# Performance work log

Hardware: AMD Instinct MI355X
Metric: run time of the kernel (lower is better)

Reference implementation:

```python
import jax, jax.numpy as jnp
import numpy as np

B, N, C, IN, H, G, OUT = 128, 256, 4, 64, 128, 8, 1
NUM_GNN_LAYERS = 2  # num_layers - 1


def setup_inputs() -> dict:
    key = jax.random.key(0)
    k1, k2, k3, k4, k5, k6 = jax.random.split(key, 6)
    V = jax.random.normal(k1, (B, N, IN), dtype=jnp.float32)
    A = jax.random.uniform(k2, (B, N, C, N), dtype=jnp.float32)
    mol_size = jax.random.randint(k3, (B,), 16, N + 1)  # at least 16 real nodes
    W_in = jax.random.normal(k4, (2, H, IN, G), dtype=jnp.float32) / np.float32(np.sqrt(IN) * np.sqrt(G))
    W_g = jax.random.normal(k5, (NUM_GNN_LAYERS, 2, H, H, G), dtype=jnp.float32) / np.float32(np.sqrt(H) * np.sqrt(G))
    W_out = jax.random.normal(k6, (2, OUT, H, 1), dtype=jnp.float32) / np.float32(np.sqrt(H))
    b_out = jnp.zeros((1, OUT), dtype=jnp.float32)
    return {"V": V, "A": A, "mol_size": mol_size, "W_in": W_in, "W_g": W_g, "W_out": W_out, "b_out": b_out}


def _kan_linear(x, W, bias=None):
    # x: [..., in], W: [2, out, in, grid]
    g = W.shape[-1]
    k = jnp.arange(1, g + 1, dtype=x.dtype)  # [g]
    xk = x[..., None] * k                    # [..., in, g]
    y = jnp.einsum('...ik,oik->...o', jnp.cos(xk), W[0]) \
      + jnp.einsum('...ik,oik->...o', jnp.sin(xk), W[1])
    if bias is not None:
        y = y + bias
    return y


def _kan_gnn_layer(h, A, W):
    # h: [b,n,in], A: [b,n,c,m], W: [2,out,in,grid]
    g = W.shape[-1]
    k = jnp.arange(1, g + 1, dtype=h.dtype)
    xk = h[..., None] * k                      # [b,n,in,g]
    f = jnp.einsum('bnik,oik->bno', jnp.cos(xk), W[0]) \
      + jnp.einsum('bnik,oik->bno', jnp.sin(xk), W[1])  # fourier_feat [b,n,out]
    # torch chain permute/reshape/bmm/sum(c) == sum_{n,c} A[b,n,c,m] * f[b,n,o]
    return jnp.einsum('bncm,bno->bmo', A, f)   # [b,m,out]


def reference(V, A, mol_size, W_in, W_g, W_out, b_out):
    h = _kan_linear(V, W_in)                   # [B,N,H]
    for i in range(W_g.shape[0]):
        m = _kan_gnn_layer(h, A, W_g[i])
        h = jax.nn.leaky_relu(m + h, negative_slope=0.01)
    # avg pooling over the first mol_size[i] (real) nodes per graph
    node_mask = (jnp.arange(N) < mol_size[:, None]).astype(h.dtype)  # [B,N]
    summed = jnp.einsum('bnh,bn->bh', h, node_mask)
    y = summed / mol_size[:, None].astype(h.dtype)                    # [B,H]
    out = jax.nn.sigmoid(_kan_linear(y, W_out, b_out))                # [B,OUT]
    return out
```

## Files before the change

### kernel.cpp

```cpp
#include <hip/hip_runtime.h>
#include <math.h>

namespace {
constexpr int B_ = 128;
constexpr int N_ = 256;
constexpr int H_ = 128;
constexpr int M_TOTAL = B_ * N_;
}

#define AS1 __attribute__((address_space(1)))
#define AS3 __attribute__((address_space(3)))

__device__ __forceinline__ void gl_lds16(const float* g, float* l) {
  __builtin_amdgcn_global_load_lds((const AS1 unsigned int*)g,
                                   (AS3 unsigned int*)l, 16, 0, 0);
}

template<int I, int O>
__global__ __launch_bounds__(256)
void wtr_kernel(const float* __restrict__ in, float* __restrict__ out) {
  int idx = blockIdx.x * 256 + threadIdx.x;
  constexpr int TOTAL = 2 * O * I * 8;
  if (idx >= TOTAL) return;
  int g = idx & 7;
  int t = idx >> 3;
  int i = t % I;
  int t2 = t / I;
  int o = t2 % O;
  int s = t2 / O;
  out[(size_t)((i * 8 + g) * 2 + s) * O + o] = in[idx];
}

__global__ __launch_bounds__(256)
void add4_kernel(const float* __restrict__ a, const float* __restrict__ b,
                 float* __restrict__ o, int n4) {
  int i = blockIdx.x * 256 + threadIdx.x;
  int stride = gridDim.x * 256;
  for (; i < n4; i += stride) {
    float4 x = ((const float4*)a)[i];
    float4 y = ((const float4*)b)[i];
    float4 r = {x.x + y.x, x.y + y.y, x.z + y.z, x.w + y.w};
    ((float4*)o)[i] = r;
  }
}

template<int IN>
__global__ __launch_bounds__(256, 4)
void fourier4(const float* __restrict__ x,
              const float* __restrict__ Wt,
              float* __restrict__ out0,
              float* __restrict__ out1)
{
  constexpr int HP = IN * 4;
  constexpr int CHUNKS = HP / 8;
  __shared__ alignas(16) float wl[2][8][2][128];
  __shared__ alignas(16) float fC[2][8][64];
  __shared__ alignas(16) float fS[2][8][64];

  const int tid = threadIdx.x;
  const int khalf = blockIdx.x & 1;
  const int node0 = (blockIdx.x >> 1) * 64;
  const int og = tid & 15;
  const int ng = tid >> 4;
  const int lane = tid & 63;
  const int wave = tid >> 6;
  const int nd = tid & 63;

  float* __restrict__ out = khalf ? out1 : out0;
  const float* wb = Wt + (size_t)khalf * HP * 256;
  const float* xrow = x + (size_t)(node0 + nd) * IN + khalf * (IN / 2);

  float acc[4][8];
  #pragma unroll
  for (int a = 0; a < 4; ++a)
    #pragma unroll
    for (int b = 0; b < 8; ++b) acc[a][b] = 0.f;

  float xv = xrow[0];
  float xnext = (CHUNKS > 1) ? xrow[1] : 0.f;
  #pragma unroll
  for (int q = 0; q < 2; ++q) {
    int bw = wave * 2 + q;
    gl_lds16(wb + (size_t)(bw * 64 + lane) * 4, &wl[0][0][0][0] + bw * 256);
  }
  {
    float s1, c1;
    sincosf(xv, &s1, &c1);
    float ckm = 1.f, skm = 0.f, ck = c1, sk = s1;
    #pragma unroll
    for (int g = 0; g < 8; ++g) {
      if ((g >> 1) == wave) { fC[0][g][nd] = ck; fS[0][g][nd] = sk; }
      float cn = 2.f * c1 * ck - ckm, sn = 2.f * c1 * sk - skm;
      ckm = ck; skm = sk; ck = cn; sk = sn;
    }
  }
  __syncthreads();

  int p = 0;
  for (int ic = 0; ic < CHUNKS; ++ic) {
    const int pn = p ^ 1;
    const bool more = (ic + 1 < CHUNKS);
    if (more) {
      const float* wsrc = wb + (size_t)(ic + 1) * 2048;
      #pragma unroll
      for (int q = 0; q < 2; ++q) {
        int bw = wave * 2 + q;
        gl_lds16(wsrc + (size_t)(bw * 64 + lane) * 4,
                 &wl[pn][0][0][0] + bw * 256);
      }
      float s1, c1;
      sincosf(xnext, &s1, &c1);
      float ckm = 1.f, skm = 0.f, ck = c1, sk = s1;
      #pragma unroll
      for (int g = 0; g < 8; ++g) {
        if ((g >> 1) == wave) { fC[pn][g][nd] = ck; fS[pn][g][nd] = sk; }
        float cn = 2.f * c1 * ck - ckm, sn = 2.f * c1 * sk - skm;
        ckm = ck; skm = sk; ck = cn; sk = sn;
      }
      if (ic + 2 < CHUNKS) xnext = xrow[ic + 2];
    }
    #pragma unroll 4
    for (int j = 0; j < 8; ++j) {
      float4 fc = *(const float4*)&fC[p][j][ng * 4];
      float4 fs = *(const float4*)&fS[p][j][ng * 4];
      float4 w0a = *(const float4*)&wl[p][j][0][og * 4];
      float4 w0b = *(const float4*)&wl[p][j][0][og * 4 + 64];
      float4 w1a = *(const float4*)&wl[p][j][1][og * 4];
      float4 w1b = *(const float4*)&wl[p][j][1][og * 4 + 64];
      float fcv[4] = {fc.x, fc.y, fc.z, fc.w};
      float fsv[4] = {fs.x, fs.y, fs.z, fs.w};
      float wa0[4] = {w0a.x, w0a.y, w0a.z, w0a.w};
      float wb0[4] = {w0b.x, w0b.y, w0b.z, w0b.w};
      float wa1[4] = {w1a.x, w1a.y, w1a.z, w1a.w};
      float wb1[4] = {w1b.x, w1b.y, w1b.z, w1b.w};
      #pragma unroll
      for (int nd2 = 0; nd2 < 4; ++nd2) {
        #pragma unroll
        for (int oo = 0; oo < 4; ++oo) {
          acc[nd2][oo]     += fcv[nd2] * wa0[oo] + fsv[nd2] * wa1[oo];
          acc[nd2][4 + oo] += fcv[nd2] * wb0[oo] + fsv[nd2] * wb1[oo];
        }
      }
    }
    __syncthreads();
    p ^= 1;
  }

  #pragma unroll
  for (int nd2 = 0; nd2 < 4; ++nd2) {
    int row = node0 + ng * 4 + nd2;
    float4 ra = {acc[nd2][0], acc[nd2][1], acc[nd2][2], acc[nd2][3]};
    float4 rb = {acc[nd2][4], acc[nd2][5], acc[nd2][6], acc[nd2][7]};
    *(float4*)&out[(size_t)row * H_ + og * 4] = ra;
    *(float4*)&out[(size_t)row * H_ + og * 4 + 64] = rb;
  }
}

__global__ __launch_bounds__(256)
void agg3(const float* __restrict__ A,
          const float* __restrict__ f0,
          const float* __restrict__ f1,
          const float* __restrict__ h_in,
          float* __restrict__ h_out)
{
  __shared__ alignas(16) float As[2][32][64];
  __shared__ alignas(16) float fsh[2][8][128];
  const int tid = threadIdx.x;
  const int b = blockIdx.x >> 2;
  const int m0 = (blockIdx.x & 3) * 64;
  const int og = tid & 15;
  const int mg = tid >> 4;
  const int wave = tid >> 6;
  const int fr = tid >> 5;
  const int fc4 = (tid & 31) * 4;

  float acc[4][8];
  #pragma unroll
  for (int i = 0; i < 4; ++i)
    #pragma unroll
    for (int j = 0; j < 8; ++j) acc[i][j] = 0.f;

  const float* Ab  = A  + (size_t)b * (N_ * 4 * N_) + m0;
  const float* f0b = f0 + (size_t)b * (N_ * H_);
  const float* f1b = f1 + (size_t)b * (N_ * H_);

  float4 u0 = *(const float4*)(f0b + (size_t)fr * H_ + fc4);
  float4 u1 = *(const float4*)(f1b + (size_t)fr * H_ + fc4);
  #pragma unroll
  for (int q = 0; q < 2; ++q) {
    int v = q * 256 + tid;
    gl_lds16(Ab + (size_t)(v >> 4) * N_ + (v & 15) * 4,
             &As[0][0][0] + (size_t)(q * 256 + wave * 64) * 4);
  }
  {
    float4 s = {u0.x + u1.x, u0.y + u1.y, u0.z + u1.z, u0.w + u1.w};
    *(float4*)&fsh[0][fr][fc4] = s;
  }
  __syncthreads();

  int p = 0;
  for (int ch = 0; ch < 32; ++ch) {
    const int pn = p ^ 1;
    float4 v0, v1;
    if (ch + 1 < 32) {
      v0 = *(const float4*)(f0b + (size_t)((ch + 1) * 8 + fr) * H_ + fc4);
      v1 = *(const float4*)(f1b + (size_t)((ch + 1) * 8 + fr) * H_ + fc4);
      const float* Asrc = Ab + (size_t)(ch + 1) * 32 * N_;
      #pragma unroll
      for (int q = 0; q < 2; ++q) {
        int v = q * 256 + tid;
        gl_lds16(Asrc + (size_t)(v >> 4) * N_ + (v & 15) * 4,
                 &As[pn][0][0] + (size_t)(q * 256 + wave * 64) * 4);
      }
    }
    #pragma unroll
    for (int kk = 0; kk < 32; ++kk) {
      float4 a  = *(const float4*)&As[p][kk][mg * 4];
      float4 g0 = *(const float4*)&fsh[p][kk >> 2][og * 4];
      float4 g1 = *(const float4*)&fsh[p][kk >> 2][og * 4 + 64];
      float av[4] = {a.x, a.y, a.z, a.w};
      float fo[8] = {g0.x, g0.y, g0.z, g0.w, g1.x, g1.y, g1.z, g1.w};
      #pragma unroll
      for (int mi = 0; mi < 4; ++mi)
        #pragma unroll
        for (int oi = 0; oi < 8; ++oi)
          acc[mi][oi] += av[mi] * fo[oi];
    }
    if (ch + 1 < 32) {
      float4 s = {v0.x + v1.x, v0.y + v1.y, v0.z + v1.z, v0.w + v1.w};
      *(float4*)&fsh[pn][fr][fc4] = s;
    }
    __syncthreads();
    p ^= 1;
  }

  #pragma unroll
  for (int mi = 0; mi < 4; ++mi) {
    int row = b * N_ + m0 + mg * 4 + mi;
    const float* hr = &h_in[(size_t)row * H_];
    float* ho = &h_out[(size_t)row * H_];
    float4 r0 = *(const float4*)&hr[og * 4];
    float4 r1 = *(const float4*)&hr[og * 4 + 64];
    float4 o0, o1;
    float v;
    v = acc[mi][0] + r0.x; o0.x = v >= 0.f ? v : 0.01f * v;
    v = acc[mi][1] + r0.y; o0.y = v >= 0.f ? v : 0.01f * v;
    v = acc[mi][2] + r0.z; o0.z = v >= 0.f ? v : 0.01f * v;
    v = acc[mi][3] + r0.w; o0.w = v >= 0.f ? v : 0.01f * v;
    v = acc[mi][4] + r1.x; o1.x = v >= 0.f ? v : 0.01f * v;
    v = acc[mi][5] + r1.y; o1.y = v >= 0.f ? v : 0.01f * v;
    v = acc[mi][6] + r1.z; o1.z = v >= 0.f ? v : 0.01f * v;
    v = acc[mi][7] + r1.w; o1.w = v >= 0.f ? v : 0.01f * v;
    *(float4*)&ho[og * 4] = o0;
    *(float4*)&ho[og * 4 + 64] = o1;
  }
}

__global__ __launch_bounds__(128)
void pool_kernel(const float* __restrict__ h,
                 const int* __restrict__ mol,
                 const float* __restrict__ Wout,
                 const float* __restrict__ bout,
                 float* __restrict__ out)
{
  __shared__ float red[128];
  const int b = blockIdx.x;
  const int t = threadIdx.x;
  const int ms = mol[b];
  const float* hb = h + (size_t)b * N_ * H_;
  float sum = 0.f;
  for (int n = 0; n < ms; ++n) sum += hb[(size_t)n * H_ + t];
  float y = sum / (float)ms;
  float s1, c1;
  sincosf(y, &s1, &c1);
  red[t] = c1 * Wout[t] + s1 * Wout[H_ + t];
  __syncthreads();
  for (int sft = 64; sft > 0; sft >>= 1) {
    if (t < sft) red[t] += red[t + sft];
    __syncthreads();
  }
  if (t == 0) {
    float z = red[0] + bout[0];
    out[b] = 1.f / (1.f + expf(-z));
  }
}

extern "C" void kernel_launch(void* const* d_in, const int* in_sizes, int n_in,
                              void* d_out, int out_size, void* d_ws, size_t ws_size,
                              hipStream_t stream) {
  const float* V    = (const float*)d_in[0];
  const float* A    = (const float*)d_in[1];
  const int*   mol  = (const int*)d_in[2];
  const float* Win  = (const float*)d_in[3];
  const float* Wg   = (const float*)d_in[4];
  const float* Wout = (const float*)d_in[5];
  const float* bout = (const float*)d_in[6];
  float* out = (float*)d_out;

  const size_t BUF = (size_t)M_TOTAL * H_;
  float* h     = (float*)d_ws;
  float* h2    = h  + BUF;
  float* f0    = h2 + BUF;
  float* f1    = f0 + BUF;
  float* wt_in = f1 + BUF;
  float* wt_g0 = wt_in + 512 * 2 * H_;
  float* wt_g1 = wt_g0 + 1024 * 2 * H_;

  wtr_kernel<64, 128><<<(2 * 128 * 64 * 8) / 256, 256, 0, stream>>>(Win, wt_in);
  wtr_kernel<128, 128><<<(2 * 128 * 128 * 8) / 256, 256, 0, stream>>>(Wg, wt_g0);
  wtr_kernel<128, 128><<<(2 * 128 * 128 * 8) / 256, 256, 0, stream>>>(
      Wg + (size_t)2 * 128 * 128 * 8, wt_g1);

  fourier4<64><<<(M_TOTAL / 64) * 2, 256, 0, stream>>>(V, wt_in, f0, f1);
  add4_kernel<<<2048, 256, 0, stream>>>(f0, f1, h, (int)(BUF / 4));

  float* hc = h;
  float* hn = h2;
  const float* wt_g[2] = {wt_g0, wt_g1};
  for (int l = 0; l < 2; ++l) {
    fourier4<128><<<(M_TOTAL / 64) * 2, 256, 0, stream>>>(hc, wt_g[l], f0, f1);
    agg3<<<B_ * 4, 256, 0, stream>>>(A, f0, f1, hc, hn);
    float* tmp = hc; hc = hn; hn = tmp;
  }

  pool_kernel<<<B_, 128, 0, stream>>>(hc, mol, Wout, bout, out);
}
```

Measured before the change: 1.006 ms.

## Enlarge per-thread register tiles to 8x8 in fourier and aggregation kernels

The Fourier feature GEMM kernel now covers 128 nodes per block, giving each thread an 8x8 accumulator tile instead of 4x8. Feature generation is split across two thread halves, with the upper half reaching harmonic 5 through angle doubling. The aggregation kernel uses 128 threads per block, and each thread computes 8 rows by 8 outputs, reusing each loaded f vector across four A rows. The goal is fewer LDS loads per FMA, at the cost of higher register pressure and lower occupancy (launch bounds 3 and 2).

```diff
diff --git a/kernel.cpp b/kernel.cpp
--- a/kernel.cpp
+++ b/kernel.cpp
@@ -45,100 +45,107 @@
 }
 
 template<int IN>
-__global__ __launch_bounds__(256, 4)
-void fourier4(const float* __restrict__ x,
+__global__ __launch_bounds__(256, 3)
+void fourier6(const float* __restrict__ x,
               const float* __restrict__ Wt,
               float* __restrict__ out0,
               float* __restrict__ out1)
 {
-  constexpr int HP = IN * 4;
-  constexpr int CHUNKS = HP / 8;
+  constexpr int HIN = IN / 2;
   __shared__ alignas(16) float wl[2][8][2][128];
-  __shared__ alignas(16) float fC[2][8][64];
-  __shared__ alignas(16) float fS[2][8][64];
+  __shared__ alignas(16) float fC[2][8][128];
+  __shared__ alignas(16) float fS[2][8][128];
 
   const int tid = threadIdx.x;
   const int khalf = blockIdx.x & 1;
-  const int node0 = (blockIdx.x >> 1) * 64;
+  const int node0 = (blockIdx.x >> 1) * 128;
   const int og = tid & 15;
   const int ng = tid >> 4;
   const int lane = tid & 63;
   const int wave = tid >> 6;
-  const int nd = tid & 63;
+  const int fnode = tid & 127;
+  const int fhi = tid >> 7;
 
   float* __restrict__ out = khalf ? out1 : out0;
-  const float* wb = Wt + (size_t)khalf * HP * 256;
-  const float* xrow = x + (size_t)(node0 + nd) * IN + khalf * (IN / 2);
-
-  float acc[4][8];
-  #pragma unroll
-  for (int a = 0; a < 4; ++a)
+  const float* wb = Wt + (size_t)khalf * HIN * 2048;
+  const float* xrow = x + (size_t)(node0 + fnode) * IN + khalf * HIN;
+
+  float acc[8][8];
+  #pragma unroll
+  for (int a = 0; a < 8; ++a)
     #pragma unroll
     for (int b = 0; b < 8; ++b) acc[a][b] = 0.f;
 
+  auto put_feats = [&](int pb, float xx) {
+    float s1, c1;
+    sincosf(xx, &s1, &c1);
+    float ck, sk;
+    if (fhi == 0) {
+      ck = c1; sk = s1;
+    } else {
+      float c2 = c1 * c1 - s1 * s1, s2 = 2.f * c1 * s1;
+      float c4 = c2 * c2 - s2 * s2, s4 = 2.f * s2 * c2;
+      ck = c4 * c1 - s4 * s1;
+      sk = s4 * c1 + c4 * s1;
+    }
+    const int g0 = fhi * 4;
+    #pragma unroll
+    for (int t = 0; t < 4; ++t) {
+      fC[pb][g0 + t][fnode] = ck;
+      fS[pb][g0 + t][fnode] = sk;
+      float cn = ck * c1 - sk * s1;
+      sk = sk * c1 + ck * s1;
+      ck = cn;
+    }
+  };
+
+  #pragma unroll
+  for (int q = 0; q < 2; ++q) {
+    int u = q * 256 + tid;
+    gl_lds16(wb + (size_t)u * 4,
+             &wl[0][0][0][0] + (size_t)(q * 256 + wave * 64) * 4);
+  }
   float xv = xrow[0];
-  float xnext = (CHUNKS > 1) ? xrow[1] : 0.f;
-  #pragma unroll
-  for (int q = 0; q < 2; ++q) {
-    int bw = wave * 2 + q;
-    gl_lds16(wb + (size_t)(bw * 64 + lane) * 4, &wl[0][0][0][0] + bw * 256);
-  }
-  {
-    float s1, c1;
-    sincosf(xv, &s1, &c1);
-    float ckm = 1.f, skm = 0.f, ck = c1, sk = s1;
-    #pragma unroll
-    for (int g = 0; g < 8; ++g) {
-      if ((g >> 1) == wave) { fC[0][g][nd] = ck; fS[0][g][nd] = sk; }
-      float cn = 2.f * c1 * ck - ckm, sn = 2.f * c1 * sk - skm;
-      ckm = ck; skm = sk; ck = cn; sk = sn;
-    }
-  }
+  float xnext = (HIN > 1) ? xrow[1] : 0.f;
+  put_feats(0, xv);
   __syncthreads();
 
   int p = 0;
-  for (int ic = 0; ic < CHUNKS; ++ic) {
+  for (int ic = 0; ic < HIN; ++ic) {
     const int pn = p ^ 1;
-    const bool more = (ic + 1 < CHUNKS);
-    if (more) {
+    if (ic + 1 < HIN) {
       const float* wsrc = wb + (size_t)(ic + 1) * 2048;
       #pragma unroll
       for (int q = 0; q < 2; ++q) {
-        int bw = wave * 2 + q;
-        gl_lds16(wsrc + (size_t)(bw * 64 + lane) * 4,
-                 &wl[pn][0][0][0] + bw * 256);
-      }
-      float s1, c1;
-      sincosf(xnext, &s1, &c1);
-      float ckm = 1.f, skm = 0.f, ck = c1, sk = s1;
-      #pragma unroll
-      for (int g = 0; g < 8; ++g) {
-        if ((g >> 1) == wave) { fC[pn][g][nd] = ck; fS[pn][g][nd] = sk; }
-        float cn = 2.f * c1 * ck - ckm, sn = 2.f * c1 * sk - skm;
-        ckm = ck; skm = sk; ck = cn; sk = sn;
-      }
-      if (ic + 2 < CHUNKS) xnext = xrow[ic + 2];
-    }
-    #pragma unroll 4
+        int u = q * 256 + tid;
+        gl_lds16(wsrc + (size_t)u * 4,
+                 &wl[pn][0][0][0] + (size_t)(q * 256 + wave * 64) * 4);
+      }
+      put_feats(pn, xnext);
+      if (ic + 2 < HIN) xnext = xrow[ic + 2];
+    }
+    #pragma unroll 2
     for (int j = 0; j < 8; ++j) {
-      float4 fc = *(const float4*)&fC[p][j][ng * 4];
-      float4 fs = *(const float4*)&fS[p][j][ng * 4];
+      float4 fc0 = *(const float4*)&fC[p][j][ng * 8];
+      float4 fc1 = *(const float4*)&fC[p][j][ng * 8 + 4];
+      float4 fs0 = *(const float4*)&fS[p][j][ng * 8];
+      float4 fs1 = *(const float4*)&fS[p][j][ng * 8 + 4];
       float4 w0a = *(const float4*)&wl[p][j][0][og * 4];
       float4 w0b = *(const float4*)&wl[p][j][0][og * 4 + 64];
       float4 w1a = *(const float4*)&wl[p][j][1][og * 4];
       float4 w1b = *(const float4*)&wl[p][j][1][og * 4 + 64];
-      float fcv[4] = {fc.x, fc.y, fc.z, fc.w};
-      float fsv[4] = {fs.x, fs.y, fs.z, fs.w};
+      float fcv[8] = {fc0.x, fc0.y, fc0.z, fc0.w, fc1.x, fc1.y, fc1.z, fc1.w};
+      float fsv[8] = {fs0.x, fs0.y, fs0.z, fs0.w, fs1.x, fs1.y, fs1.z, fs1.w};
       float wa0[4] = {w0a.x, w0a.y, w0a.z, w0a.w};
       float wb0[4] = {w0b.x, w0b.y, w0b.z, w0b.w};
       float wa1[4] = {w1a.x, w1a.y, w1a.z, w1a.w};
       float wb1[4] = {w1b.x, w1b.y, w1b.z, w1b.w};
       #pragma unroll
-      for (int nd2 = 0; nd2 < 4; ++nd2) {
+      for (int nd = 0; nd < 8; ++nd) {
         #pragma unroll
         for (int oo = 0; oo < 4; ++oo) {
-          acc[nd2][oo]     += fcv[nd2] * wa0[oo] + fsv[nd2] * wa1[oo];
-          acc[nd2][4 + oo] += fcv[nd2] * wb0[oo] + fsv[nd2] * wb1[oo];
+          acc[nd][oo]     += fcv[nd] * wa0[oo] + fsv[nd] * wa1[oo];
+          acc[nd][4 + oo] += fcv[nd] * wb0[oo] + fsv[nd] * wb1[oo];
         }
       }
     }
@@ -147,17 +154,17 @@
   }
 
   #pragma unroll
-  for (int nd2 = 0; nd2 < 4; ++nd2) {
-    int row = node0 + ng * 4 + nd2;
-    float4 ra = {acc[nd2][0], acc[nd2][1], acc[nd2][2], acc[nd2][3]};
-    float4 rb = {acc[nd2][4], acc[nd2][5], acc[nd2][6], acc[nd2][7]};
+  for (int nd = 0; nd < 8; ++nd) {
+    int row = node0 + ng * 8 + nd;
+    float4 ra = {acc[nd][0], acc[nd][1], acc[nd][2], acc[nd][3]};
+    float4 rb = {acc[nd][4], acc[nd][5], acc[nd][6], acc[nd][7]};
     *(float4*)&out[(size_t)row * H_ + og * 4] = ra;
     *(float4*)&out[(size_t)row * H_ + og * 4 + 64] = rb;
   }
 }
 
-__global__ __launch_bounds__(256)
-void agg3(const float* __restrict__ A,
+__global__ __launch_bounds__(128, 2)
+void agg5(const float* __restrict__ A,
           const float* __restrict__ f0,
           const float* __restrict__ f1,
           const float* __restrict__ h_in,
@@ -171,12 +178,10 @@
   const int og = tid & 15;
   const int mg = tid >> 4;
   const int wave = tid >> 6;
-  const int fr = tid >> 5;
-  const int fc4 = (tid & 31) * 4;
-
-  float acc[4][8];
-  #pragma unroll
-  for (int i = 0; i < 4; ++i)
+
+  float acc[8][8];
+  #pragma unroll
+  for (int i = 0; i < 8; ++i)
     #pragma unroll
     for (int j = 0; j < 8; ++j) acc[i][j] = 0.f;
 
@@ -184,59 +189,83 @@
   const float* f0b = f0 + (size_t)b * (N_ * H_);
   const float* f1b = f1 + (size_t)b * (N_ * H_);
 
-  float4 u0 = *(const float4*)(f0b + (size_t)fr * H_ + fc4);
-  float4 u1 = *(const float4*)(f1b + (size_t)fr * H_ + fc4);
+  float4 u0[2], u1[2];
   #pragma unroll
   for (int q = 0; q < 2; ++q) {
-    int v = q * 256 + tid;
+    int u = q * 128 + tid;
+    u0[q] = *(const float4*)(f0b + (size_t)(u >> 5) * H_ + (u & 31) * 4);
+    u1[q] = *(const float4*)(f1b + (size_t)(u >> 5) * H_ + (u & 31) * 4);
+  }
+  #pragma unroll
+  for (int q = 0; q < 4; ++q) {
+    int v = q * 128 + tid;
     gl_lds16(Ab + (size_t)(v >> 4) * N_ + (v & 15) * 4,
-             &As[0][0][0] + (size_t)(q * 256 + wave * 64) * 4);
-  }
-  {
-    float4 s = {u0.x + u1.x, u0.y + u1.y, u0.z + u1.z, u0.w + u1.w};
-    *(float4*)&fsh[0][fr][fc4] = s;
+             &As[0][0][0] + (size_t)(q * 128 + wave * 64) * 4);
+  }
+  #pragma unroll
+  for (int q = 0; q < 2; ++q) {
+    int u = q * 128 + tid;
+    float4 s = {u0[q].x + u1[q].x, u0[q].y + u1[q].y,
+                u0[q].z + u1[q].z, u0[q].w + u1[q].w};
+    *(float4*)&fsh[0][u >> 5][(u & 31) * 4] = s;
   }
   __syncthreads();
 
   int p = 0;
   for (int ch = 0; ch < 32; ++ch) {
     const int pn = p ^ 1;
-    float4 v0, v1;
+    float4 v0[2], v1[2];
     if (ch + 1 < 32) {
-      v0 = *(const float4*)(f0b + (size_t)((ch + 1) * 8 + fr) * H_ + fc4);
-      v1 = *(const float4*)(f1b + (size_t)((ch + 1) * 8 + fr) * H_ + fc4);
+      #pragma unroll
+      for (int q = 0; q < 2; ++q) {
+        int u = q * 128 + tid;
+        v0[q] = *(const float4*)(f0b +
+                   (size_t)((ch + 1) * 8 + (u >> 5)) * H_ + (u & 31) * 4);
+        v1[q] = *(const float4*)(f1b +
+                   (size_t)((ch + 1) * 8 + (u >> 5)) * H_ + (u & 31) * 4);
+      }
       const float* Asrc = Ab + (size_t)(ch + 1) * 32 * N_;
       #pragma unroll
+      for (int q = 0; q < 4; ++q) {
+        int v = q * 128 + tid;
+        gl_lds16(Asrc + (size_t)(v >> 4) * N_ + (v & 15) * 4,
+                 &As[pn][0][0] + (size_t)(q * 128 + wave * 64) * 4);
+      }
+    }
+    #pragma unroll 2
+    for (int q8 = 0; q8 < 8; ++q8) {
+      float4 g0 = *(const float4*)&fsh[p][q8][og * 4];
+      float4 g1 = *(const float4*)&fsh[p][q8][og * 4 + 64];
+      float fo[8] = {g0.x, g0.y, g0.z, g0.w, g1.x, g1.y, g1.z, g1.w};
+      #pragma unroll
+      for (int k4 = 0; k4 < 4; ++k4) {
+        int kk = q8 * 4 + k4;
+        float4 a0 = *(const float4*)&As[p][kk][mg * 8];
+        float4 a1 = *(const float4*)&As[p][kk][mg * 8 + 4];
+        float am[8] = {a0.x, a0.y, a0.z, a0.w, a1.x, a1.y, a1.z, a1.w};
+        #pragma unroll
+        for (int mi = 0; mi < 8; ++mi)
+          #pragma unroll
+          for (int oi = 0; oi < 8; ++oi)
+            acc[mi][oi] += am[mi] * fo[oi];
+      }
+    }
+    if (ch + 1 < 32) {
+      #pragma unroll
       for (int q = 0; q < 2; ++q) {
-        int v = q * 256 + tid;
-        gl_lds16(Asrc + (size_t)(v >> 4) * N_ + (v & 15) * 4,
-                 &As[pn][0][0] + (size_t)(q * 256 + wave * 64) * 4);
-      }
-    }
-    #pragma unroll
-    for (int kk = 0; kk < 32; ++kk) {
-      float4 a  = *(const float4*)&As[p][kk][mg * 4];
-      float4 g0 = *(const float4*)&fsh[p][kk >> 2][og * 4];
-      float4 g1 = *(const float4*)&fsh[p][kk >> 2][og * 4 + 64];
-      float av[4] = {a.x, a.y, a.z, a.w};
-      float fo[8] = {g0.x, g0.y, g0.z, g0.w, g1.x, g1.y, g1.z, g1.w};
-      #pragma unroll
-      for (int mi = 0; mi < 4; ++mi)
-        #pragma unroll
-        for (int oi = 0; oi < 8; ++oi)
-          acc[mi][oi] += av[mi] * fo[oi];
-    }
-    if (ch + 1 < 32) {
-      float4 s = {v0.x + v1.x, v0.y + v1.y, v0.z + v1.z, v0.w + v1.w};
-      *(float4*)&fsh[pn][fr][fc4] = s;
+        int u = q * 128 + tid;
+        float4 s = {v0[q].x + v1[q].x, v0[q].y + v1[q].y,
+                    v0[q].z + v1[q].z, v0[q].w + v1[q].w};
+        *(float4*)&fsh[pn][u >> 5][(u & 31) * 4] = s;
+      }
     }
     __syncthreads();
     p ^= 1;
   }
 
   #pragma unroll
-  for (int mi = 0; mi < 4; ++mi) {
-    int row = b * N_ + m0 + mg * 4 + mi;
+  for (int mi = 0; mi < 8; ++mi) {
+    int row = b * N_ + m0 + mg * 8 + mi;
     const float* hr = &h_in[(size_t)row * H_];
     float* ho = &h_out[(size_t)row * H_];
     float4 r0 = *(const float4*)&hr[og * 4];
@@ -311,15 +340,15 @@
   wtr_kernel<128, 128><<<(2 * 128 * 128 * 8) / 256, 256, 0, stream>>>(
       Wg + (size_t)2 * 128 * 128 * 8, wt_g1);
 
-  fourier4<64><<<(M_TOTAL / 64) * 2, 256, 0, stream>>>(V, wt_in, f0, f1);
+  fourier6<64><<<(M_TOTAL / 128) * 2, 256, 0, stream>>>(V, wt_in, f0, f1);
   add4_kernel<<<2048, 256, 0, stream>>>(f0, f1, h, (int)(BUF / 4));
 
   float* hc = h;
   float* hn = h2;
   const float* wt_g[2] = {wt_g0, wt_g1};
   for (int l = 0; l < 2; ++l) {
-    fourier4<128><<<(M_TOTAL / 64) * 2, 256, 0, stream>>>(hc, wt_g[l], f0, f1);
-    agg3<<<B_ * 4, 256, 0, stream>>>(A, f0, f1, hc, hn);
+    fourier6<128><<<(M_TOTAL / 128) * 2, 256, 0, stream>>>(hc, wt_g[l], f0, f1);
+    agg5<<<B_ * 4, 128, 0, stream>>>(A, f0, f1, hc, hn);
     float* tmp = hc; hc = hn; hn = tmp;
   }
 
```

After: 1.076 ms. 6.9% more time.
